# Kernel optimization log

Hardware: AMD Instinct MI355X
Metric: run time of the kernel (lower is better)

## Reference

```python
import jax, jax.numpy as jnp
import numpy as np

B, S, E = 4, 2048, 1024
H = 16
D = E // H  # head_size = 64


def setup_inputs() -> dict:
    key = jax.random.key(0)
    k1, k2, k3 = jax.random.split(key, 3)
    scale = 0.02
    return {
        "x": jax.random.normal(k1, (B, S, E), dtype=jnp.float32),
        "w_qkv": jax.random.normal(k2, (E, 3 * E), dtype=jnp.float32) * scale,
        "b_qkv": jnp.zeros((3 * E,), dtype=jnp.float32),
        "w_proj": jax.random.normal(k3, (E, E), dtype=jnp.float32) * scale,
        "b_proj": jnp.zeros((E,), dtype=jnp.float32),
    }


def reference(x, w_qkv, b_qkv, w_proj, b_proj):
    bsz, seq_len, embd = x.shape
    qkv = x @ w_qkv + b_qkv                              # [B,S,3E]
    q, k, v = jnp.split(qkv, 3, axis=2)
    # [B,S,E] -> [B,H,S,D]
    q = q.reshape(bsz, seq_len, H, D).transpose(0, 2, 1, 3)
    k = k.reshape(bsz, seq_len, H, D).transpose(0, 2, 1, 3)
    v = v.reshape(bsz, seq_len, H, D).transpose(0, 2, 1, 3)
    att = jnp.einsum("bhqd,bhkd->bhqk", q, k) / jnp.sqrt(jnp.float32(D))
    causal = jnp.tril(jnp.ones((seq_len, seq_len), dtype=bool))
    att = jnp.where(causal[None, None, :, :], att, -jnp.inf)
    att = jax.nn.softmax(att, axis=-1)
    y = jnp.einsum("bhqk,bhkd->bhqd", att, v)            # [B,H,S,D]
    y = y.transpose(0, 2, 1, 3).reshape(bsz, seq_len, embd)
    return y @ w_proj + b_proj
```

## Files before the change

### kernel.cpp

```cpp
#include <hip/hip_runtime.h>
#include <cmath>
#include <cstdint>

#define BB 4
#define SS 2048
#define EE 1024
#define HH 16
#define DD 64
#define ROWS (BB*SS)
#define QKV_N (3*EE)
#define NQT 16

using bf16x8 = __attribute__((ext_vector_type(8))) __bf16;
using bf16x4 = __attribute__((ext_vector_type(4))) __bf16;
using f32x4  = __attribute__((ext_vector_type(4))) float;
typedef __attribute__((ext_vector_type(4))) short short4v;

#define SCQ 0.18033688f

__device__ inline f32x4 mfma16(bf16x8 a, bf16x8 b, f32x4 c) {
    return __builtin_amdgcn_mfma_f32_16x16x32_bf16(a, b, c, 0, 0, 0);
}

__device__ inline f32x4 mfma16k16(bf16x4 a, bf16x4 b, f32x4 c) {
    return __builtin_amdgcn_mfma_f32_16x16x16bf16_1k(
        __builtin_bit_cast(short4v, a), __builtin_bit_cast(short4v, b), c, 0, 0, 0);
}

__device__ inline void load_lds16(const void* g, void* l) {
    __builtin_amdgcn_global_load_lds(
        (__attribute__((address_space(1))) void*)g,
        (__attribute__((address_space(3))) void*)l, 16, 0, 0);
}

__global__ __launch_bounds__(256) void cast_f32_bf16(const float* __restrict__ in,
                                                     __bf16* __restrict__ out) {
    size_t i = ((size_t)blockIdx.x * 256 + threadIdx.x) * 4;
    float4 v = *(const float4*)(in + i);
    bf16x4 o;
    o[0] = (__bf16)v.x; o[1] = (__bf16)v.y; o[2] = (__bf16)v.z; o[3] = (__bf16)v.w;
    *(bf16x4*)(out + i) = o;
}

__global__ __launch_bounds__(256) void transpose_cast(const float* __restrict__ in,
                                                      __bf16* __restrict__ out,
                                                      int K, int N) {
    __shared__ float tile[32][33];
    int n0 = blockIdx.x * 32, k0 = blockIdx.y * 32;
    int tx = threadIdx.x, ty = threadIdx.y;
#pragma unroll
    for (int i = 0; i < 4; ++i)
        tile[ty + 8 * i][tx] = in[(size_t)(k0 + ty + 8 * i) * N + n0 + tx];
    __syncthreads();
#pragma unroll
    for (int i = 0; i < 4; ++i)
        out[(size_t)(n0 + ty + 8 * i) * K + k0 + tx] = (__bf16)tile[tx][ty + 8 * i];
}

__global__ __launch_bounds__(256) void build_vt(const __bf16* __restrict__ qkv,
                                                __bf16* __restrict__ vt) {
    __shared__ __bf16 tile[64 * 72];
    const int s0 = blockIdx.x * 64, h = blockIdx.y, b = blockIdx.z;
    const int tid = threadIdx.x;
#pragma unroll
    for (int r = 0; r < 2; ++r) {
        int c = r * 256 + tid;
        int s = c >> 3, dp = c & 7;
        bf16x8 v = *(const bf16x8*)(qkv + (size_t)(b * SS + s0 + s) * QKV_N + 2048 + h * 64 + dp * 8);
        *(bf16x8*)(tile + s * 72 + dp * 8) = v;
    }
    __syncthreads();
#pragma unroll
    for (int r = 0; r < 2; ++r) {
        int c = r * 256 + tid;
        int d = c >> 3, sp = c & 7;
        bf16x8 o;
#pragma unroll
        for (int i = 0; i < 8; ++i) o[i] = tile[(sp * 8 + i) * 72 + d];
        *(bf16x8*)(vt + (size_t)((b * HH + h) * 64 + d) * SS + s0 + sp * 8) = o;
    }
}

template <bool OUT_BF16, bool QSCALE>
__global__ __launch_bounds__(256) void gemm_bt(const __bf16* __restrict__ A,
                                               const __bf16* __restrict__ Bt,
                                               const float* __restrict__ bias,
                                               void* __restrict__ Cout,
                                               int M, int N, int K) {
    __shared__ __bf16 As[128 * 32];
    __shared__ __bf16 Bs[128 * 32];
    const int tid  = threadIdx.x;
    const int wave = tid >> 6;
    const int lane = tid & 63;
    const int lrow = lane & 15;
    const int quad = lane >> 4;
    const int wm   = (wave >> 1) * 64;
    const int wn   = (wave & 1) * 64;
    const int tm   = blockIdx.x * 128;
    const int tn   = blockIdx.y * 128;

    f32x4 acc[4][4] = {};

    const int srow = lane >> 2;
    const int skoff = (lane & 3) * 8;

    for (int k0 = 0; k0 < K; k0 += 32) {
        __syncthreads();
#pragma unroll
        for (int i = 0; i < 2; ++i) {
            int c = wave * 2 + i;
            int row = 16 * c + srow;
            load_lds16(A + (size_t)(tm + row) * K + k0 + skoff, As + c * 512);
            load_lds16(Bt + (size_t)(tn + row) * K + k0 + skoff, Bs + c * 512);
        }
        __syncthreads();

        bf16x8 bfr[4];
#pragma unroll
        for (int ni = 0; ni < 4; ++ni)
            bfr[ni] = *(const bf16x8*)(Bs + (wn + ni * 16 + lrow) * 32 + quad * 8);
#pragma unroll
        for (int mi = 0; mi < 4; ++mi) {
            bf16x8 a = *(const bf16x8*)(As + (wm + mi * 16 + lrow) * 32 + quad * 8);
#pragma unroll
            for (int ni = 0; ni < 4; ++ni)
                acc[mi][ni] = mfma16(a, bfr[ni], acc[mi][ni]);
        }
    }

#pragma unroll
    for (int ni = 0; ni < 4; ++ni) {
        int cn = tn + wn + ni * 16 + lrow;
        float bv = bias[cn];
        float sc = (QSCALE && cn < EE) ? SCQ : 1.0f;
#pragma unroll
        for (int mi = 0; mi < 4; ++mi) {
#pragma unroll
            for (int r = 0; r < 4; ++r) {
                int gm = tm + wm + mi * 16 + quad * 4 + r;
                float v = (acc[mi][ni][r] + bv) * sc;
                if (OUT_BF16)
                    ((__bf16*)Cout)[(size_t)gm * N + cn] = (__bf16)v;
                else
                    ((float*)Cout)[(size_t)gm * N + cn] = v;
            }
        }
    }
}

__device__ __forceinline__ void stage_kv(const __bf16* __restrict__ kbase,
                                         const __bf16* __restrict__ vbase,
                                         __bf16* Kb, __bf16* Vb, int kb, int tid) {
#pragma unroll
    for (int r = 0; r < 4; ++r) {
        int c = r * 256 + tid;
        int row = c >> 3;
        int g8 = ((c & 7) ^ (row & 7)) * 8;
        load_lds16(kbase + (size_t)(kb + row) * QKV_N + g8, Kb + c * 8);
    }
#pragma unroll
    for (int r = 0; r < 4; ++r) {
        int c = r * 256 + tid;
        int d = c >> 4, kc = c & 15;
        int g8 = ((kc & 8) | ((kc & 7) ^ (d & 7))) * 8;
        load_lds16(vbase + (size_t)d * SS + kb + g8, Vb + c * 8);
    }
}

__global__ __launch_bounds__(256) void attn7(const __bf16* __restrict__ qkv,
                                             const __bf16* __restrict__ vt,
                                             __bf16* __restrict__ y) {
    const int hb = blockIdx.x;
    const int h = hb & 15, b = hb >> 4;
    const int j = blockIdx.y;
    const int tid = threadIdx.x;
    const int wave = tid >> 6, lane = tid & 63;
    const int lrow = lane & 15, quad = lane >> 4;

    __shared__ __bf16 Klds[2][128 * 64];
    __shared__ __bf16 Vlds[2][64 * 128];

    const __bf16* kbase = qkv + (size_t)b * SS * QKV_N + 1024 + h * 64;
    const __bf16* vbase = vt + (size_t)(b * HH + h) * 64 * SS;

    const int qtA = NQT - 1 - j, qtB = j;
    const int nA = qtA + 1, total = nA + qtB + 1;

    stage_kv(kbase, vbase, Klds[0], Vlds[0], 0, tid);

    int it = 0;
    for (int seg = 0; seg < 2; ++seg) {
        const int qtile = seg ? qtB : qtA;
        const int qbase = qtile * 128;

        bf16x8 qf[2][2];
#pragma unroll
        for (int g = 0; g < 2; ++g) {
            const __bf16* qp = qkv + (size_t)(b * SS + qbase + 64 * g + wave * 16 + lrow) * QKV_N + h * 64;
            qf[g][0] = *(const bf16x8*)(qp + quad * 8);
            qf[g][1] = *(const bf16x8*)(qp + 32 + quad * 8);
        }
        const int q0 = qbase + wave * 16 + lrow;

        float m[2] = {-INFINITY, -INFINITY}, l[2] = {0.f, 0.f};
        f32x4 oacc[2][4] = {};

        for (int kb_i = 0; kb_i <= qtile; ++kb_i, ++it) {
            const int cur = it & 1;
            const int kb = kb_i * 128;
            const bool diag = (kb_i == qtile);
            __syncthreads();
            if (it + 1 < total) {
                int nit = it + 1;
                int nkb = (nit < nA ? nit : nit - nA) * 128;
                stage_kv(kbase, vbase, Klds[cur ^ 1], Vlds[cur ^ 1], nkb, tid);
            }
            const __bf16* Kb = Klds[cur];
            const __bf16* Vb = Vlds[cur];

#pragma unroll
            for (int ch = 0; ch < 2; ++ch) {
                const bool do0 = !(diag && ch == 1);
                f32x4 s0[4], s1[4];
#pragma unroll
                for (int t = 0; t < 4; ++t) {
                    const __bf16* kr = Kb + (64 * ch + 16 * t + lrow) * 64;
                    bf16x8 kf0 = *(const bf16x8*)(kr + 8 * (quad ^ (lrow & 7)));
                    bf16x8 kf1 = *(const bf16x8*)(kr + 8 * ((4 + quad) ^ (lrow & 7)));
                    f32x4 c1 = {};
                    c1 = mfma16(kf0, qf[1][0], c1);
                    c1 = mfma16(kf1, qf[1][1], c1);
                    s1[t] = c1;
                    if (do0) {
                        f32x4 c0 = {};
                        c0 = mfma16(kf0, qf[0][0], c0);
                        c0 = mfma16(kf1, qf[0][1], c0);
                        s0[t] = c0;
                    }
                }
                if (diag) {
                    if (ch == 0) {
#pragma unroll
                        for (int t = 0; t < 4; ++t)
#pragma unroll
                            for (int r = 0; r < 4; ++r)
                                if (kb + 16 * t + 4 * quad + r > q0) s0[t][r] = -INFINITY;
                    } else {
#pragma unroll
                        for (int t = 0; t < 4; ++t)
#pragma unroll
                            for (int r = 0; r < 4; ++r)
                                if (kb + 64 + 16 * t + 4 * quad + r > q0 + 64) s1[t][r] = -INFINITY;
                    }
                }

                bf16x4 p0[4], p1[4];
#pragma unroll
                for (int g = 0; g < 2; ++g) {
                    if (g == 0 && !do0) continue;
                    f32x4* s = g ? s1 : s0;
                    bf16x4* p = g ? p1 : p0;
                    float mx = -INFINITY;
#pragma unroll
                    for (int t = 0; t < 4; ++t)
                        mx = fmaxf(mx, fmaxf(fmaxf(s[t][0], s[t][1]), fmaxf(s[t][2], s[t][3])));
                    mx = fmaxf(mx, __shfl_xor(mx, 16));
                    mx = fmaxf(mx, __shfl_xor(mx, 32));
                    float mnew = fmaxf(m[g], mx);
                    float alpha = exp2f(m[g] - mnew);
                    m[g] = mnew;
                    float rs = 0.f;
#pragma unroll
                    for (int t = 0; t < 4; ++t) {
#pragma unroll
                        for (int r = 0; r < 4; ++r) {
                            float e = exp2f(s[t][r] - mnew);
                            rs += e;
                            p[t][r] = (__bf16)e;
                        }
                    }
                    rs += __shfl_xor(rs, 16);
                    rs += __shfl_xor(rs, 32);
                    l[g] = l[g] * alpha + rs;
#pragma unroll
                    for (int td = 0; td < 4; ++td) {
                        oacc[g][td][0] *= alpha; oacc[g][td][1] *= alpha;
                        oacc[g][td][2] *= alpha; oacc[g][td][3] *= alpha;
                    }
                }

#pragma unroll
                for (int t = 0; t < 4; ++t) {
                    int klog = 8 * ch + 2 * t + (quad >> 1);
                    int c = (klog & 8) | ((klog & 7) ^ (lrow & 7));
                    const __bf16* vcol = Vb + (size_t)lrow * 128 + c * 8 + 4 * (quad & 1);
#pragma unroll
                    for (int td = 0; td < 4; ++td) {
                        bf16x4 vf = *(const bf16x4*)(vcol + td * 16 * 128);
                        oacc[1][td] = mfma16k16(vf, p1[t], oacc[1][td]);
                        if (do0) oacc[0][td] = mfma16k16(vf, p0[t], oacc[0][td]);
                    }
                }
            }
        }

#pragma unroll
        for (int g = 0; g < 2; ++g) {
            float linv = 1.f / l[g];
            __bf16* yp = y + (size_t)(b * SS + qbase + 64 * g + wave * 16 + lrow) * EE + h * 64;
#pragma unroll
            for (int td = 0; td < 4; ++td) {
                bf16x4 o;
#pragma unroll
                for (int r = 0; r < 4; ++r) o[r] = (__bf16)(oacc[g][td][r] * linv);
                *(bf16x4*)(yp + 16 * td + 4 * quad) = o;
            }
        }
    }
}

extern "C" void kernel_launch(void* const* d_in, const int* in_sizes, int n_in,
                              void* d_out, int out_size, void* d_ws, size_t ws_size,
                              hipStream_t stream) {
    const float* x      = (const float*)d_in[0];
    const float* w_qkv  = (const float*)d_in[1];
    const float* b_qkv  = (const float*)d_in[2];
    const float* w_proj = (const float*)d_in[3];
    const float* b_proj = (const float*)d_in[4];
    float* out = (float*)d_out;

    __bf16* xb     = (__bf16*)d_ws;
    __bf16* wqkvT  = xb + (size_t)ROWS * EE;
    __bf16* wprojT = wqkvT + (size_t)QKV_N * EE;
    __bf16* qkv    = wprojT + (size_t)EE * EE;
    __bf16* yb     = qkv + (size_t)ROWS * QKV_N;
    __bf16* vtb    = xb;

    cast_f32_bf16<<<dim3(ROWS * EE / 1024), dim3(256), 0, stream>>>(x, xb);
    transpose_cast<<<dim3(QKV_N / 32, EE / 32), dim3(32, 8), 0, stream>>>(w_qkv, wqkvT, EE, QKV_N);
    transpose_cast<<<dim3(EE / 32, EE / 32), dim3(32, 8), 0, stream>>>(w_proj, wprojT, EE, EE);
    gemm_bt<true, true><<<dim3(ROWS / 128, QKV_N / 128), dim3(256), 0, stream>>>(
        xb, wqkvT, b_qkv, (void*)qkv, ROWS, QKV_N, EE);
    build_vt<<<dim3(SS / 64, HH, BB), dim3(256), 0, stream>>>(qkv, vtb);
    attn7<<<dim3(HH * BB, NQT / 2), dim3(256), 0, stream>>>(qkv, vtb, yb);
    gemm_bt<false, false><<<dim3(ROWS / 128, EE / 128), dim3(256), 0, stream>>>(
        yb, wprojT, b_proj, (void*)out, ROWS, EE, EE);
}
```

Baseline: 301.8 us.

## Fuse prep kernels and restructure attention inner loop over full 128-key tile

Merges the x cast and both weight transpose-casts into one prep launch, which removes two kernel launches. In attention, K/V staging pointers and LDS read offsets are precomputed once per block rather than recomputed on every iteration. The two 64-key chunks become a single 128-key pass with one softmax update per tile. This halves the number of max/sum reductions and rescales, but the diagonal tile now computes a fully masked half for the first query group, and the larger s/p arrays raise register pressure.

```diff
diff --git a/kernel.cpp b/kernel.cpp
--- a/kernel.cpp
+++ b/kernel.cpp
@@ -33,28 +33,44 @@
         (__attribute__((address_space(3))) void*)l, 16, 0, 0);
 }
 
-__global__ __launch_bounds__(256) void cast_f32_bf16(const float* __restrict__ in,
-                                                     __bf16* __restrict__ out) {
-    size_t i = ((size_t)blockIdx.x * 256 + threadIdx.x) * 4;
-    float4 v = *(const float4*)(in + i);
-    bf16x4 o;
-    o[0] = (__bf16)v.x; o[1] = (__bf16)v.y; o[2] = (__bf16)v.z; o[3] = (__bf16)v.w;
-    *(bf16x4*)(out + i) = o;
-}
-
-__global__ __launch_bounds__(256) void transpose_cast(const float* __restrict__ in,
-                                                      __bf16* __restrict__ out,
-                                                      int K, int N) {
+#define PREP_CAST 8192
+#define PREP_TQKV 3072
+__global__ __launch_bounds__(256) void prep(const float* __restrict__ x,
+                                            const float* __restrict__ w_qkv,
+                                            const float* __restrict__ w_proj,
+                                            __bf16* __restrict__ xb,
+                                            __bf16* __restrict__ wqkvT,
+                                            __bf16* __restrict__ wprojT) {
     __shared__ float tile[32][33];
-    int n0 = blockIdx.x * 32, k0 = blockIdx.y * 32;
-    int tx = threadIdx.x, ty = threadIdx.y;
+    const int bid = blockIdx.x, tid = threadIdx.x;
+    if (bid < PREP_CAST) {
+        size_t i = ((size_t)bid * 256 + tid) * 4;
+        float4 v = *(const float4*)(x + i);
+        bf16x4 o;
+        o[0] = (__bf16)v.x; o[1] = (__bf16)v.y; o[2] = (__bf16)v.z; o[3] = (__bf16)v.w;
+        *(bf16x4*)(xb + i) = o;
+        return;
+    }
+    const float* in;
+    __bf16* out;
+    int N, n0, k0;
+    if (bid < PREP_CAST + PREP_TQKV) {
+        int b2 = bid - PREP_CAST;
+        in = w_qkv; out = wqkvT; N = QKV_N;
+        n0 = (b2 % (QKV_N / 32)) * 32; k0 = (b2 / (QKV_N / 32)) * 32;
+    } else {
+        int b3 = bid - PREP_CAST - PREP_TQKV;
+        in = w_proj; out = wprojT; N = EE;
+        n0 = (b3 % (EE / 32)) * 32; k0 = (b3 / (EE / 32)) * 32;
+    }
+    const int tx = tid & 31, ty = tid >> 5;
 #pragma unroll
     for (int i = 0; i < 4; ++i)
         tile[ty + 8 * i][tx] = in[(size_t)(k0 + ty + 8 * i) * N + n0 + tx];
     __syncthreads();
 #pragma unroll
     for (int i = 0; i < 4; ++i)
-        out[(size_t)(n0 + ty + 8 * i) * K + k0 + tx] = (__bf16)tile[tx][ty + 8 * i];
+        out[(size_t)(n0 + ty + 8 * i) * EE + k0 + tx] = (__bf16)tile[tx][ty + 8 * i];
 }
 
 __global__ __launch_bounds__(256) void build_vt(const __bf16* __restrict__ qkv,
@@ -148,26 +164,7 @@
     }
 }
 
-__device__ __forceinline__ void stage_kv(const __bf16* __restrict__ kbase,
-                                         const __bf16* __restrict__ vbase,
-                                         __bf16* Kb, __bf16* Vb, int kb, int tid) {
-#pragma unroll
-    for (int r = 0; r < 4; ++r) {
-        int c = r * 256 + tid;
-        int row = c >> 3;
-        int g8 = ((c & 7) ^ (row & 7)) * 8;
-        load_lds16(kbase + (size_t)(kb + row) * QKV_N + g8, Kb + c * 8);
-    }
-#pragma unroll
-    for (int r = 0; r < 4; ++r) {
-        int c = r * 256 + tid;
-        int d = c >> 4, kc = c & 15;
-        int g8 = ((kc & 8) | ((kc & 7) ^ (d & 7))) * 8;
-        load_lds16(vbase + (size_t)d * SS + kb + g8, Vb + c * 8);
-    }
-}
-
-__global__ __launch_bounds__(256) void attn7(const __bf16* __restrict__ qkv,
+__global__ __launch_bounds__(256) void attn8(const __bf16* __restrict__ qkv,
                                              const __bf16* __restrict__ vt,
                                              __bf16* __restrict__ y) {
     const int hb = blockIdx.x;
@@ -183,10 +180,40 @@
     const __bf16* kbase = qkv + (size_t)b * SS * QKV_N + 1024 + h * 64;
     const __bf16* vbase = vt + (size_t)(b * HH + h) * 64 * SS;
 
+    const __bf16* kptr[4];
+    const __bf16* vptr[4];
+#pragma unroll
+    for (int r = 0; r < 4; ++r) {
+        int c = r * 256 + tid;
+        int row = c >> 3;
+        int g8 = ((c & 7) ^ (row & 7)) * 8;
+        kptr[r] = kbase + (size_t)row * QKV_N + g8;
+        int d = c >> 4, kc = c & 15;
+        int vg8 = ((kc & 8) | ((kc & 7) ^ (d & 7))) * 8;
+        vptr[r] = vbase + (size_t)d * SS + vg8;
+    }
+    const int koff0 = lrow * 64 + 8 * (quad ^ (lrow & 7));
+    const int koff1 = lrow * 64 + 8 * ((4 + quad) ^ (lrow & 7));
+    int voff[8];
+#pragma unroll
+    for (int tt = 0; tt < 8; ++tt) {
+        int klog = 2 * tt + (quad >> 1);
+        int c = (klog & 8) | ((klog & 7) ^ (lrow & 7));
+        voff[tt] = lrow * 128 + c * 8 + 4 * (quad & 1);
+    }
+
+    auto stage = [&](int kb2, __bf16* Kb, __bf16* Vb) {
+#pragma unroll
+        for (int r = 0; r < 4; ++r) {
+            load_lds16(kptr[r] + (size_t)kb2 * QKV_N, Kb + (r * 256 + tid) * 8);
+            load_lds16(vptr[r] + kb2, Vb + (r * 256 + tid) * 8);
+        }
+    };
+
     const int qtA = NQT - 1 - j, qtB = j;
     const int nA = qtA + 1, total = nA + qtB + 1;
 
-    stage_kv(kbase, vbase, Klds[0], Vlds[0], 0, tid);
+    stage(0, Klds[0], Vlds[0]);
 
     int it = 0;
     for (int seg = 0; seg < 2; ++seg) {
@@ -213,93 +240,81 @@
             if (it + 1 < total) {
                 int nit = it + 1;
                 int nkb = (nit < nA ? nit : nit - nA) * 128;
-                stage_kv(kbase, vbase, Klds[cur ^ 1], Vlds[cur ^ 1], nkb, tid);
+                stage(nkb, Klds[cur ^ 1], Vlds[cur ^ 1]);
             }
             const __bf16* Kb = Klds[cur];
             const __bf16* Vb = Vlds[cur];
 
-#pragma unroll
-            for (int ch = 0; ch < 2; ++ch) {
-                const bool do0 = !(diag && ch == 1);
-                f32x4 s0[4], s1[4];
-#pragma unroll
-                for (int t = 0; t < 4; ++t) {
-                    const __bf16* kr = Kb + (64 * ch + 16 * t + lrow) * 64;
-                    bf16x8 kf0 = *(const bf16x8*)(kr + 8 * (quad ^ (lrow & 7)));
-                    bf16x8 kf1 = *(const bf16x8*)(kr + 8 * ((4 + quad) ^ (lrow & 7)));
-                    f32x4 c1 = {};
-                    c1 = mfma16(kf0, qf[1][0], c1);
-                    c1 = mfma16(kf1, qf[1][1], c1);
-                    s1[t] = c1;
-                    if (do0) {
-                        f32x4 c0 = {};
-                        c0 = mfma16(kf0, qf[0][0], c0);
-                        c0 = mfma16(kf1, qf[0][1], c0);
-                        s0[t] = c0;
+            f32x4 s0[8], s1[8];
+#pragma unroll
+            for (int tt = 0; tt < 8; ++tt) {
+                bf16x8 kf0 = *(const bf16x8*)(Kb + tt * 1024 + koff0);
+                bf16x8 kf1 = *(const bf16x8*)(Kb + tt * 1024 + koff1);
+                f32x4 c0 = {};
+                c0 = mfma16(kf0, qf[0][0], c0);
+                c0 = mfma16(kf1, qf[0][1], c0);
+                s0[tt] = c0;
+                f32x4 c1 = {};
+                c1 = mfma16(kf0, qf[1][0], c1);
+                c1 = mfma16(kf1, qf[1][1], c1);
+                s1[tt] = c1;
+            }
+
+            if (diag) {
+#pragma unroll
+                for (int tt = 0; tt < 8; ++tt)
+#pragma unroll
+                    for (int r = 0; r < 4; ++r) {
+                        int key = kb + 16 * tt + 4 * quad + r;
+                        if (key > q0)      s0[tt][r] = -INFINITY;
+                        if (key > q0 + 64) s1[tt][r] = -INFINITY;
                     }
+            }
+
+            bf16x4 p0[8], p1[8];
+#pragma unroll
+            for (int g = 0; g < 2; ++g) {
+                f32x4* s = g ? s1 : s0;
+                bf16x4* p = g ? p1 : p0;
+                float mx = -INFINITY;
+#pragma unroll
+                for (int tt = 0; tt < 8; ++tt)
+                    mx = fmaxf(mx, fmaxf(fmaxf(s[tt][0], s[tt][1]), fmaxf(s[tt][2], s[tt][3])));
+                mx = fmaxf(mx, __shfl_xor(mx, 16));
+                mx = fmaxf(mx, __shfl_xor(mx, 32));
+                float mnew = fmaxf(m[g], mx);
+                float alpha = exp2f(m[g] - mnew);
+                m[g] = mnew;
+                float rs = 0.f;
+#pragma unroll
+                for (int tt = 0; tt < 8; ++tt) {
+                    bf16x4 pk;
+#pragma unroll
+                    for (int r = 0; r < 4; ++r) {
+                        float e = exp2f(s[tt][r] - mnew);
+                        rs += e;
+                        pk[r] = (__bf16)e;
+                    }
+                    p[tt] = pk;
                 }
-                if (diag) {
-                    if (ch == 0) {
-#pragma unroll
-                        for (int t = 0; t < 4; ++t)
-#pragma unroll
-                            for (int r = 0; r < 4; ++r)
-                                if (kb + 16 * t + 4 * quad + r > q0) s0[t][r] = -INFINITY;
-                    } else {
-#pragma unroll
-                        for (int t = 0; t < 4; ++t)
-#pragma unroll
-                            for (int r = 0; r < 4; ++r)
-                                if (kb + 64 + 16 * t + 4 * quad + r > q0 + 64) s1[t][r] = -INFINITY;
-                    }
+                rs += __shfl_xor(rs, 16);
+                rs += __shfl_xor(rs, 32);
+                l[g] = l[g] * alpha + rs;
+#pragma unroll
+                for (int td = 0; td < 4; ++td) {
+                    oacc[g][td][0] *= alpha; oacc[g][td][1] *= alpha;
+                    oacc[g][td][2] *= alpha; oacc[g][td][3] *= alpha;
                 }
-
-                bf16x4 p0[4], p1[4];
-#pragma unroll
-                for (int g = 0; g < 2; ++g) {
-                    if (g == 0 && !do0) continue;
-                    f32x4* s = g ? s1 : s0;
-                    bf16x4* p = g ? p1 : p0;
-                    float mx = -INFINITY;
-#pragma unroll
-                    for (int t = 0; t < 4; ++t)
-                        mx = fmaxf(mx, fmaxf(fmaxf(s[t][0], s[t][1]), fmaxf(s[t][2], s[t][3])));
-                    mx = fmaxf(mx, __shfl_xor(mx, 16));
-                    mx = fmaxf(mx, __shfl_xor(mx, 32));
-                    float mnew = fmaxf(m[g], mx);
-                    float alpha = exp2f(m[g] - mnew);
-                    m[g] = mnew;
-                    float rs = 0.f;
-#pragma unroll
-                    for (int t = 0; t < 4; ++t) {
-#pragma unroll
-                        for (int r = 0; r < 4; ++r) {
-                            float e = exp2f(s[t][r] - mnew);
-                            rs += e;
-                            p[t][r] = (__bf16)e;
-                        }
-                    }
-                    rs += __shfl_xor(rs, 16);
-                    rs += __shfl_xor(rs, 32);
-                    l[g] = l[g] * alpha + rs;
-#pragma unroll
-                    for (int td = 0; td < 4; ++td) {
-                        oacc[g][td][0] *= alpha; oacc[g][td][1] *= alpha;
-                        oacc[g][td][2] *= alpha; oacc[g][td][3] *= alpha;
-                    }
-                }
-
-#pragma unroll
-                for (int t = 0; t < 4; ++t) {
-                    int klog = 8 * ch + 2 * t + (quad >> 1);
-                    int c = (klog & 8) | ((klog & 7) ^ (lrow & 7));
-                    const __bf16* vcol = Vb + (size_t)lrow * 128 + c * 8 + 4 * (quad & 1);
-#pragma unroll
-                    for (int td = 0; td < 4; ++td) {
-                        bf16x4 vf = *(const bf16x4*)(vcol + td * 16 * 128);
-                        oacc[1][td] = mfma16k16(vf, p1[t], oacc[1][td]);
-                        if (do0) oacc[0][td] = mfma16k16(vf, p0[t], oacc[0][td]);
-                    }
+            }
+
+#pragma unroll
+            for (int tt = 0; tt < 8; ++tt) {
+                const __bf16* vc = Vb + voff[tt];
+#pragma unroll
+                for (int td = 0; td < 4; ++td) {
+                    bf16x4 vf = *(const bf16x4*)(vc + td * 2048);
+                    oacc[0][td] = mfma16k16(vf, p0[tt], oacc[0][td]);
+                    oacc[1][td] = mfma16k16(vf, p1[tt], oacc[1][td]);
                 }
             }
         }
@@ -336,13 +351,12 @@
     __bf16* yb     = qkv + (size_t)ROWS * QKV_N;
     __bf16* vtb    = xb;
 
-    cast_f32_bf16<<<dim3(ROWS * EE / 1024), dim3(256), 0, stream>>>(x, xb);
-    transpose_cast<<<dim3(QKV_N / 32, EE / 32), dim3(32, 8), 0, stream>>>(w_qkv, wqkvT, EE, QKV_N);
-    transpose_cast<<<dim3(EE / 32, EE / 32), dim3(32, 8), 0, stream>>>(w_proj, wprojT, EE, EE);
+    prep<<<dim3(PREP_CAST + PREP_TQKV + EE * EE / 1024), dim3(256), 0, stream>>>(
+        x, w_qkv, w_proj, xb, wqkvT, wprojT);
     gemm_bt<true, true><<<dim3(ROWS / 128, QKV_N / 128), dim3(256), 0, stream>>>(
         xb, wqkvT, b_qkv, (void*)qkv, ROWS, QKV_N, EE);
     build_vt<<<dim3(SS / 64, HH, BB), dim3(256), 0, stream>>>(qkv, vtb);
-    attn7<<<dim3(HH * BB, NQT / 2), dim3(256), 0, stream>>>(qkv, vtb, yb);
+    attn8<<<dim3(HH * BB, NQT / 2), dim3(256), 0, stream>>>(qkv, vtb, yb);
     gemm_bt<false, false><<<dim3(ROWS / 128, EE / 128), dim3(256), 0, stream>>>(
         yb, wprojT, b_proj, (void*)out, ROWS, EE, EE);
 }
```

After: 318.3 us. 1.05x slower.
